# Performance work log

Measured on AMD Instinct MI355X. Metric: run time of the kernel, lower is better.

The kernel has to match this reference:

```python
import jax, jax.numpy as jnp
import numpy as np

NUM_EMBEDDINGS = 512
EMBEDDING_DIM = 64
COMMITMENT_COST = 0.25


def setup_inputs() -> dict:
    key = jax.random.key(0)
    k1, k2 = jax.random.split(key)
    inputs = jax.random.normal(k1, (32, EMBEDDING_DIM, 64, 64), dtype=jnp.float32)
    # embedding.weight ~ U(-1/num_embeddings, 1/num_embeddings)
    codebook = jax.random.uniform(
        k2, (NUM_EMBEDDINGS, EMBEDDING_DIM), dtype=jnp.float32,
        minval=-1.0 / NUM_EMBEDDINGS, maxval=1.0 / NUM_EMBEDDINGS)
    return {"inputs": inputs, "codebook": codebook}


def reference(inputs, codebook):
    B, C, H, W = inputs.shape  # C == embedding_dim
    # NCHW -> (B*H*W, C)
    flat = inputs.transpose(0, 2, 3, 1).reshape(-1, C)
    # squared euclidean distances to each codebook entry: [N, K]
    distances = (
        jnp.sum(flat ** 2, axis=1, keepdims=True)
        - 2.0 * jnp.matmul(flat, codebook.T)
        + jnp.sum(codebook ** 2, axis=1)[None, :]
    )
    encoding_indices = jnp.argmin(distances, axis=1)  # [N]
    # gather == one-hot @ codebook, same math, no dense one-hot
    quantized = jnp.take(codebook, encoding_indices, axis=0)
    quantized = quantized.reshape(B, H, W, C).transpose(0, 3, 1, 2)
    e_latent_loss = jnp.mean((jax.lax.stop_gradient(quantized) - inputs) ** 2)
    q_latent_loss = jnp.mean((quantized - jax.lax.stop_gradient(inputs)) ** 2)
    loss = q_latent_loss + COMMITMENT_COST * e_latent_loss
    # straight-through estimator
    quantized_st = inputs + jax.lax.stop_gradient(quantized - inputs)
    return (quantized_st, loss)
```

## Files before the change

### kernel.cpp

```cpp
#include <hip/hip_runtime.h>


#define NUM_EMB 512
#define DIM     64
#define HW      4096
#define NPIX    131072
#define NELEM   8388608.0f
#define MARGIN  6e-5f
#define LIST_CAP 65536

typedef __attribute__((ext_vector_type(8))) short bf16x8;
typedef __attribute__((ext_vector_type(4))) float f32x4;

#define WS_BFRAG 0
#define WS_EN2   131072
#define WS_IDX   133120
#define WS_BS1   395264
#define WS_CNT   397312
#define WS_LIST  397328

__device__ __forceinline__ unsigned short bf16_rne(float f) {
    unsigned int u = __float_as_uint(f);
    unsigned int r = u + 0x7FFFu + ((u >> 16) & 1u);
    return (unsigned short)(r >> 16);
}
__device__ __forceinline__ float bf16_to_f32(unsigned short h) {
    return __uint_as_float(((unsigned int)h) << 16);
}

__global__ void vq_setup(const float* __restrict__ cb, float* __restrict__ ws)
{
    const int tid = threadIdx.x;
    const int c   = blockIdx.x;
    if (c == 0 && tid == 0) *(unsigned int*)((char*)ws + WS_CNT) = 0u;
    if (c == 0) {
        float* en2s = ws + WS_EN2 / 4;
        for (int k = tid; k < NUM_EMB; k += 256) {
            const float4* row = (const float4*)(cb + k * DIM);
            float s = 0.f;
#pragma unroll
            for (int c4 = 0; c4 < DIM / 4; ++c4) {
                float4 e = row[c4];
                s += e.x * e.x + e.y * e.y + e.z * e.z + e.w * e.w;
            }
            en2s[k] = s;
        }
    }
    unsigned int* bf = (unsigned int*)ws;
    const int lane = tid & 63;
    const int quad = tid >> 6;
    const int ks = quad >> 1, h = quad & 1;
    const int code = c * 16 + (lane & 15);
    const int dg = (lane >> 4) * 8;
    unsigned int outw[4];
#pragma unroll
    for (int j2 = 0; j2 < 4; ++j2) {
        unsigned short halves[2];
#pragma unroll
        for (int t = 0; t < 2; ++t) {
            const int j = j2 * 2 + t;
            const int dim = ks * 32 + dg + j;
            const float v = -2.0f * cb[code * DIM + dim];
            const unsigned short vh = bf16_rne(v);
            const float lo = v - bf16_to_f32(vh);
            const unsigned short vl = bf16_rne(lo);
            halves[t] = h ? vl : vh;
        }
        outw[j2] = (unsigned int)halves[0] | ((unsigned int)halves[1] << 16);
    }
    unsigned int* dst = bf + (((c * 2 + ks) * 2 + h) * 64 + lane) * 4;
    dst[0] = outw[0]; dst[1] = outw[1]; dst[2] = outw[2]; dst[3] = outw[3];
}

__global__ __launch_bounds__(256, 4) void vq_mfma(
    const float* __restrict__ x, float* __restrict__ ws)
{
    const float* en2s = ws + WS_EN2 / 4;
    const uint4* bf   = (const uint4*)ws;
    unsigned short* idxb = (unsigned short*)((char*)ws + WS_IDX);
    unsigned int* cntp = (unsigned int*)((char*)ws + WS_CNT);
    unsigned int* list = (unsigned int*)((char*)ws + WS_LIST);

    __shared__ float en2l[NUM_EMB];
    for (int i = threadIdx.x; i < NUM_EMB; i += 256) en2l[i] = en2s[i];
    __syncthreads();

    const int l   = threadIdx.x & 63;
    const int w   = threadIdx.x >> 6;
    const int pwb = blockIdx.x * 128 + w * 32;
    const int b   = pwb >> 12;
    const int hwb = (pwb & 4095) + (l & 15);
    const int dg  = (l >> 4) * 8;
    const float* xb = x + (size_t)b * (DIM * HW);

    bf16x8 ah[2][2], al[2][2];
#pragma unroll
    for (int t = 0; t < 2; ++t)
#pragma unroll
        for (int ks = 0; ks < 2; ++ks)
#pragma unroll
            for (int j = 0; j < 8; ++j) {
                const int d = ks * 32 + dg + j;
                const float v = xb[(size_t)d * HW + hwb + t * 16];
                const unsigned short vh = bf16_rne(v);
                const float lo = v - bf16_to_f32(vh);
                ah[t][ks][j] = (short)vh;
                al[t][ks][j] = (short)bf16_rne(lo);
            }

    float m1[8], m2[8]; int i1[8];
#pragma unroll
    for (int s = 0; s < 8; ++s) { m1[s] = 3.4e38f; m2[s] = 3.4e38f; i1[s] = 0; }

    const int mycol = l & 15;
#define MFMA_B __builtin_amdgcn_mfma_f32_16x16x32_bf16

    uint4 cb0, cb1, cb2, cb3;
    cb0 = bf[0 * 256 + 0 * 128 + 0 * 64 + l];
    cb1 = bf[0 * 256 + 1 * 128 + 0 * 64 + l];
    cb2 = bf[0 * 256 + 0 * 128 + 1 * 64 + l];
    cb3 = bf[0 * 256 + 1 * 128 + 1 * 64 + l];

    for (int c = 0; c < 32; ++c) {
        uint4 nb0, nb1, nb2, nb3;
        if (c < 31) {
            nb0 = bf[(c + 1) * 256 + 0 * 128 + 0 * 64 + l];
            nb1 = bf[(c + 1) * 256 + 1 * 128 + 0 * 64 + l];
            nb2 = bf[(c + 1) * 256 + 0 * 128 + 1 * 64 + l];
            nb3 = bf[(c + 1) * 256 + 1 * 128 + 1 * 64 + l];
        }
        const bf16x8 bh0 = __builtin_bit_cast(bf16x8, cb0);
        const bf16x8 bh1 = __builtin_bit_cast(bf16x8, cb1);
        const bf16x8 bl0 = __builtin_bit_cast(bf16x8, cb2);
        const bf16x8 bl1 = __builtin_bit_cast(bf16x8, cb3);
        const float ev = en2l[c * 16 + mycol];

        f32x4 acc[2];
#pragma unroll
        for (int t = 0; t < 2; ++t) acc[t] = (f32x4){ev, ev, ev, ev};
#pragma unroll
        for (int t = 0; t < 2; ++t) acc[t] = MFMA_B(ah[t][0], bh0, acc[t], 0, 0, 0);
#pragma unroll
        for (int t = 0; t < 2; ++t) acc[t] = MFMA_B(ah[t][1], bh1, acc[t], 0, 0, 0);
#pragma unroll
        for (int t = 0; t < 2; ++t) acc[t] = MFMA_B(al[t][0], bh0, acc[t], 0, 0, 0);
#pragma unroll
        for (int t = 0; t < 2; ++t) acc[t] = MFMA_B(al[t][1], bh1, acc[t], 0, 0, 0);
#pragma unroll
        for (int t = 0; t < 2; ++t) acc[t] = MFMA_B(ah[t][0], bl0, acc[t], 0, 0, 0);
#pragma unroll
        for (int t = 0; t < 2; ++t) acc[t] = MFMA_B(ah[t][1], bl1, acc[t], 0, 0, 0);

#pragma unroll
        for (int t = 0; t < 2; ++t)
#pragma unroll
            for (int r = 0; r < 4; ++r) {
                const int s = t * 4 + r;
                const float v = acc[t][r];
                const bool lt = v < m1[s];
                m2[s] = fminf(m2[s], fmaxf(m1[s], v));
                i1[s] = lt ? (c * 16 + mycol) : i1[s];
                m1[s] = fminf(m1[s], v);
            }
        cb0 = nb0; cb1 = nb1; cb2 = nb2; cb3 = nb3;
    }

#pragma unroll
    for (int s = 0; s < 8; ++s) {
        float a1 = m1[s], a2 = m2[s]; int ai = i1[s];
#pragma unroll
        for (int off = 1; off < 16; off <<= 1) {
            const float b1 = __shfl_xor(a1, off);
            const float b2 = __shfl_xor(a2, off);
            const int   bi = __shfl_xor(ai, off);
            a2 = fminf(fminf(a2, b2), fmaxf(a1, b1));
            const bool take = (b1 < a1) || ((b1 == a1) && (bi < ai));
            ai = take ? bi : ai;
            a1 = fminf(a1, b1);
        }
        m1[s] = a1; m2[s] = a2; i1[s] = ai;
    }

    if ((l & 15) == 0) {
        const int g = l >> 4;
#pragma unroll
        for (int t = 0; t < 2; ++t)
#pragma unroll
            for (int r = 0; r < 4; ++r) {
                const int s = t * 4 + r;
                const int p = pwb + t * 16 + g * 4 + r;
                unsigned short v = (unsigned short)i1[s];
                if ((m2[s] - m1[s]) <= MARGIN) {
                    const unsigned int slot = atomicAdd(cntp, 1u);
                    if (slot < LIST_CAP) { list[slot] = (unsigned int)p; v = 0xFFFFu; }
                }
                idxb[p] = v;
            }
    }
}

__global__ __launch_bounds__(64) void vq_fixup(
    const float* __restrict__ x, const float* __restrict__ cb,
    float* __restrict__ ws)
{
    const float* en2s = ws + WS_EN2 / 4;
    unsigned short* idxb = (unsigned short*)((char*)ws + WS_IDX);
    const unsigned int* list = (const unsigned int*)((const char*)ws + WS_LIST);
    unsigned int cnt = *(const unsigned int*)((const char*)ws + WS_CNT);
    if (cnt > LIST_CAP) cnt = LIST_CAP;

    const int l = threadIdx.x;
    for (unsigned int wi = blockIdx.x; wi < cnt; wi += gridDim.x) {
        const int p  = (int)list[wi];
        const int b  = p >> 12;
        const int hw = p & 4095;
        const float xv = x[(size_t)b * (DIM * HW) + (size_t)l * HW + hw];
        float xsq = 0.f;
        for (int c = 0; c < DIM; ++c) {
            const float xc = __shfl(xv, c);
            xsq = fmaf(xc, xc, xsq);
        }
        float ch0[8], ch1[8], ch2[8], ch3[8];
#pragma unroll
        for (int s = 0; s < 8; ++s) { ch0[s] = ch1[s] = ch2[s] = ch3[s] = 0.f; }
        for (int c4 = 0; c4 < DIM / 4; ++c4) {
            const float x0 = __shfl(xv, 4 * c4 + 0);
            const float x1 = __shfl(xv, 4 * c4 + 1);
            const float x2 = __shfl(xv, 4 * c4 + 2);
            const float x3 = __shfl(xv, 4 * c4 + 3);
#pragma unroll
            for (int s = 0; s < 8; ++s) {
                const float4 e = *(const float4*)(cb + (l * 8 + s) * DIM + 4 * c4);
                ch0[s] = fmaf(x0, e.x, ch0[s]);
                ch1[s] = fmaf(x1, e.y, ch1[s]);
                ch2[s] = fmaf(x2, e.z, ch2[s]);
                ch3[s] = fmaf(x3, e.w, ch3[s]);
            }
        }
        float best = 3.4e38f; int bidx = 0;
#pragma unroll
        for (int s = 0; s < 8; ++s) {
            const float dot = (ch0[s] + ch1[s]) + (ch2[s] + ch3[s]);
            const float dist = fmaf(-2.f, dot, xsq) + en2s[l * 8 + s];
            if (dist < best) { best = dist; bidx = l * 8 + s; }
        }
#pragma unroll
        for (int off = 1; off < 64; off <<= 1) {
            const float bv = __shfl_xor(best, off);
            const int   bi = __shfl_xor(bidx, off);
            const bool take = (bv < best) || ((bv == best) && (bi < bidx));
            bidx = take ? bi : bidx;
            best = fminf(best, bv);
        }
        if (l == 0) idxb[p] = (unsigned short)bidx;
    }
}

__global__ __launch_bounds__(256, 2) void vq_epilogue(
    const float* __restrict__ x, const float* __restrict__ cb,
    float* __restrict__ out, float* __restrict__ ws)
{
    const unsigned short* idxb = (const unsigned short*)((const char*)ws + WS_IDX);
    float* bs1 = ws + WS_BS1 / 4;
    __shared__ float wsum[4];

    const int p  = blockIdx.x * 256 + threadIdx.x;
    const int b  = p >> 12;
    const int hw = p & 4095;
    const float* xp = x + (size_t)b * (DIM * HW) + hw;
    float* op       = out + (size_t)b * (DIM * HW) + hw;

    const int f = (int)idxb[p];
    const float4* qrow = (const float4*)(cb + f * DIM);
    float lsum = 0.f;
#pragma unroll
    for (int c4 = 0; c4 < DIM / 4; ++c4) {
        const float4 e = qrow[c4];
        const float x0 = xp[(size_t)(4 * c4 + 0) * HW];
        const float x1 = xp[(size_t)(4 * c4 + 1) * HW];
        const float x2 = xp[(size_t)(4 * c4 + 2) * HW];
        const float x3 = xp[(size_t)(4 * c4 + 3) * HW];
        const float dx0 = e.x - x0, dx1 = e.y - x1;
        const float dx2 = e.z - x2, dx3 = e.w - x3;
        op[(size_t)(4 * c4 + 0) * HW] = x0 + dx0;
        op[(size_t)(4 * c4 + 1) * HW] = x1 + dx1;
        op[(size_t)(4 * c4 + 2) * HW] = x2 + dx2;
        op[(size_t)(4 * c4 + 3) * HW] = x3 + dx3;
        lsum = fmaf(dx0, dx0, lsum);
        lsum = fmaf(dx1, dx1, lsum);
        lsum = fmaf(dx2, dx2, lsum);
        lsum = fmaf(dx3, dx3, lsum);
    }
#pragma unroll
    for (int off = 32; off > 0; off >>= 1)
        lsum += __shfl_xor(lsum, off);
    const int wid = threadIdx.x >> 6;
    if ((threadIdx.x & 63) == 0) wsum[wid] = lsum;
    __syncthreads();
    if (threadIdx.x == 0)
        bs1[blockIdx.x] = (wsum[0] + wsum[1]) + (wsum[2] + wsum[3]);
}

__global__ void vq_final(float* __restrict__ ws, float* __restrict__ lossp)
{
    const float* bs1 = ws + WS_BS1 / 4;
    float v = bs1[threadIdx.x];
#pragma unroll
    for (int off = 32; off > 0; off >>= 1)
        v += __shfl_xor(v, off);
    __shared__ float wsh[8];
    const int wid = threadIdx.x >> 6;
    if ((threadIdx.x & 63) == 0) wsh[wid] = v;
    __syncthreads();
    if (threadIdx.x == 0) {
        float s = 0.f;
#pragma unroll
        for (int i = 0; i < 8; ++i) s += wsh[i];
        const float L = s / NELEM;
        *lossp = L + 0.25f * L;
    }
}

extern "C" void kernel_launch(void* const* d_in, const int* in_sizes, int n_in,
                              void* d_out, int out_size, void* d_ws, size_t ws_size,
                              hipStream_t stream)
{
    const float* x  = (const float*)d_in[0];
    const float* cb = (const float*)d_in[1];
    float* out      = (float*)d_out;
    float* wsf      = (float*)d_ws;

    vq_setup   <<<32,   256, 0, stream>>>(cb, wsf);
    vq_mfma    <<<1024, 256, 0, stream>>>(x, wsf);
    vq_fixup   <<<2048,  64, 0, stream>>>(x, cb, wsf);
    vq_epilogue<<<512,  256, 0, stream>>>(x, cb, out, wsf);
    vq_final   <<<1,    512, 0, stream>>>(wsf, out + (size_t)NPIX * DIM);
}
```

Baseline: 172.4 us.

## Stage codebook fragments in shared memory and fold final loss reduction into epilogue

In the main MFMA kernel, each block now cooperatively loads each codebook chunk once into a double-buffered LDS array, one uint4 per thread, and synchronizes every iteration. Before, every wave loaded all four fragments from global memory itself. The running second-minimum update is replaced with a single fmed3 instruction. The separate single-block final-reduction kernel is removed: the last epilogue block, picked by an atomic ticket counter, sums the per-block partials. This saves one kernel launch but adds thread fences and an atomic per block.

```diff
diff --git a/kernel.cpp b/kernel.cpp
--- a/kernel.cpp
+++ b/kernel.cpp
@@ -32,7 +32,7 @@
 {
     const int tid = threadIdx.x;
     const int c   = blockIdx.x;
-    if (c == 0 && tid == 0) *(unsigned int*)((char*)ws + WS_CNT) = 0u;
+    if (c == 0 && tid < 2) ((unsigned int*)((char*)ws + WS_CNT))[tid] = 0u;
     if (c == 0) {
         float* en2s = ws + WS_EN2 / 4;
         for (int k = tid; k < NUM_EMB; k += 256) {
@@ -76,17 +76,21 @@
     const float* __restrict__ x, float* __restrict__ ws)
 {
     const float* en2s = ws + WS_EN2 / 4;
-    const uint4* bf   = (const uint4*)ws;
+    const uint4* bfg  = (const uint4*)ws;
     unsigned short* idxb = (unsigned short*)((char*)ws + WS_IDX);
     unsigned int* cntp = (unsigned int*)((char*)ws + WS_CNT);
     unsigned int* list = (unsigned int*)((char*)ws + WS_LIST);
 
+    __shared__ uint4 bbuf[2][256];
     __shared__ float en2l[NUM_EMB];
-    for (int i = threadIdx.x; i < NUM_EMB; i += 256) en2l[i] = en2s[i];
-    __syncthreads();
-
-    const int l   = threadIdx.x & 63;
-    const int w   = threadIdx.x >> 6;
+
+    const int tid = threadIdx.x;
+    for (int i = tid; i < NUM_EMB; i += 256) en2l[i] = en2s[i];
+
+    uint4 st0 = bfg[tid];
+
+    const int l   = tid & 63;
+    const int w   = tid >> 6;
     const int pwb = blockIdx.x * 128 + w * 32;
     const int b   = pwb >> 12;
     const int hwb = (pwb & 4095) + (l & 15);
@@ -108,6 +112,9 @@
                 al[t][ks][j] = (short)bf16_rne(lo);
             }
 
+    bbuf[0][tid] = st0;
+    __syncthreads();
+
     float m1[8], m2[8]; int i1[8];
 #pragma unroll
     for (int s = 0; s < 8; ++s) { m1[s] = 3.4e38f; m2[s] = 3.4e38f; i1[s] = 0; }
@@ -115,24 +122,16 @@
     const int mycol = l & 15;
 #define MFMA_B __builtin_amdgcn_mfma_f32_16x16x32_bf16
 
-    uint4 cb0, cb1, cb2, cb3;
-    cb0 = bf[0 * 256 + 0 * 128 + 0 * 64 + l];
-    cb1 = bf[0 * 256 + 1 * 128 + 0 * 64 + l];
-    cb2 = bf[0 * 256 + 0 * 128 + 1 * 64 + l];
-    cb3 = bf[0 * 256 + 1 * 128 + 1 * 64 + l];
-
+#pragma unroll 2
     for (int c = 0; c < 32; ++c) {
-        uint4 nb0, nb1, nb2, nb3;
-        if (c < 31) {
-            nb0 = bf[(c + 1) * 256 + 0 * 128 + 0 * 64 + l];
-            nb1 = bf[(c + 1) * 256 + 1 * 128 + 0 * 64 + l];
-            nb2 = bf[(c + 1) * 256 + 0 * 128 + 1 * 64 + l];
-            nb3 = bf[(c + 1) * 256 + 1 * 128 + 1 * 64 + l];
-        }
-        const bf16x8 bh0 = __builtin_bit_cast(bf16x8, cb0);
-        const bf16x8 bh1 = __builtin_bit_cast(bf16x8, cb1);
-        const bf16x8 bl0 = __builtin_bit_cast(bf16x8, cb2);
-        const bf16x8 bl1 = __builtin_bit_cast(bf16x8, cb3);
+        const int cur = c & 1;
+        uint4 stn;
+        if (c < 31) stn = bfg[(c + 1) * 256 + tid];
+
+        const bf16x8 bh0 = __builtin_bit_cast(bf16x8, bbuf[cur][0 * 64 + l]);
+        const bf16x8 bl0 = __builtin_bit_cast(bf16x8, bbuf[cur][1 * 64 + l]);
+        const bf16x8 bh1 = __builtin_bit_cast(bf16x8, bbuf[cur][2 * 64 + l]);
+        const bf16x8 bl1 = __builtin_bit_cast(bf16x8, bbuf[cur][3 * 64 + l]);
         const float ev = en2l[c * 16 + mycol];
 
         f32x4 acc[2];
@@ -158,11 +157,13 @@
                 const int s = t * 4 + r;
                 const float v = acc[t][r];
                 const bool lt = v < m1[s];
-                m2[s] = fminf(m2[s], fmaxf(m1[s], v));
+                m2[s] = __builtin_amdgcn_fmed3f(m1[s], m2[s], v);
                 i1[s] = lt ? (c * 16 + mycol) : i1[s];
                 m1[s] = fminf(m1[s], v);
             }
-        cb0 = nb0; cb1 = nb1; cb2 = nb2; cb3 = nb3;
+
+        if (c < 31) bbuf[cur ^ 1][tid] = stn;
+        __syncthreads();
     }
 
 #pragma unroll
@@ -258,11 +259,13 @@
 
 __global__ __launch_bounds__(256, 2) void vq_epilogue(
     const float* __restrict__ x, const float* __restrict__ cb,
-    float* __restrict__ out, float* __restrict__ ws)
+    float* __restrict__ out, float* __restrict__ ws, float* __restrict__ lossp)
 {
     const unsigned short* idxb = (const unsigned short*)((const char*)ws + WS_IDX);
     float* bs1 = ws + WS_BS1 / 4;
+    unsigned int* ticketp = (unsigned int*)((char*)ws + WS_CNT) + 1;
     __shared__ float wsum[4];
+    __shared__ unsigned int ticket_s;
 
     const int p  = blockIdx.x * 256 + threadIdx.x;
     const int b  = p >> 12;
@@ -299,25 +302,30 @@
     __syncthreads();
     if (threadIdx.x == 0)
         bs1[blockIdx.x] = (wsum[0] + wsum[1]) + (wsum[2] + wsum[3]);
-}
-
-__global__ void vq_final(float* __restrict__ ws, float* __restrict__ lossp)
-{
-    const float* bs1 = ws + WS_BS1 / 4;
-    float v = bs1[threadIdx.x];
-#pragma unroll
-    for (int off = 32; off > 0; off >>= 1)
-        v += __shfl_xor(v, off);
-    __shared__ float wsh[8];
-    const int wid = threadIdx.x >> 6;
-    if ((threadIdx.x & 63) == 0) wsh[wid] = v;
+
+    __threadfence();
+    if (threadIdx.x == 0) ticket_s = atomicAdd(ticketp, 1u);
     __syncthreads();
-    if (threadIdx.x == 0) {
-        float s = 0.f;
-#pragma unroll
-        for (int i = 0; i < 8; ++i) s += wsh[i];
-        const float L = s / NELEM;
-        *lossp = L + 0.25f * L;
+    if (ticket_s == 511) {
+        __threadfence();
+        const int t = threadIdx.x;
+        float v0 = bs1[t];
+        float v1 = bs1[t + 256];
+#pragma unroll
+        for (int off = 32; off > 0; off >>= 1) {
+            v0 += __shfl_xor(v0, off);
+            v1 += __shfl_xor(v1, off);
+        }
+        __shared__ float wsh[8];
+        if ((t & 63) == 0) { wsh[t >> 6] = v0; wsh[(t >> 6) + 4] = v1; }
+        __syncthreads();
+        if (t == 0) {
+            float s = 0.f;
+#pragma unroll
+            for (int i = 0; i < 8; ++i) s += wsh[i];
+            const float L = s / NELEM;
+            *lossp = L + 0.25f * L;
+        }
     }
 }
 
@@ -333,6 +341,6 @@
     vq_setup   <<<32,   256, 0, stream>>>(cb, wsf);
     vq_mfma    <<<1024, 256, 0, stream>>>(x, wsf);
     vq_fixup   <<<2048,  64, 0, stream>>>(x, cb, wsf);
-    vq_epilogue<<<512,  256, 0, stream>>>(x, cb, out, wsf);
-    vq_final   <<<1,    512, 0, stream>>>(wsf, out + (size_t)NPIX * DIM);
-}
+    vq_epilogue<<<512,  256, 0, stream>>>(x, cb, out, wsf,
+                                          out + (size_t)NPIX * DIM);
+}
```

Measured after the change: 251.7 us. 46.0% more time.
